# Performance work log

Measured on AMD Instinct MI355X. Metric: run time of the kernel, lower is better.

## Reference

```python
import jax, jax.numpy as jnp
import numpy as np

N_IN = 1024
N_OUT = 1024
BATCH = 8192
N_GRID = 10  # grid_points = linspace(-1, 1, 10); 9 segments
LN_EPS = 1e-5


def setup_inputs() -> dict:
    key = jax.random.key(0)
    k = jax.random.split(key, 6)
    return {
        "x": jax.random.normal(k[0], (BATCH, N_IN), dtype=jnp.float32),
        "weights": jax.random.normal(k[1], (N_OUT, N_IN), dtype=jnp.float32) * (1.0 / np.sqrt(N_IN)),
        "biases": jax.random.normal(k[2], (N_OUT,), dtype=jnp.float32),
        "slopes": jax.random.normal(k[3], (N_OUT, N_IN, N_GRID - 1), dtype=jnp.float32) * 0.05,
        "intercepts": jax.random.normal(k[4], (N_OUT, N_IN, N_GRID - 1), dtype=jnp.float32) * 0.05,
        "prelu_weight": jnp.full((1,), 0.25, dtype=jnp.float32),
    }


def reference(x, weights, biases, slopes, intercepts, prelu_weight):
    grid = jnp.linspace(-1.0, 1.0, N_GRID, dtype=x.dtype)
    n_seg = N_GRID - 1

    # base branch: GELU (exact, matching torch nn.GELU default) then linear
    b_out = jax.nn.gelu(x, approximate=False) @ weights.T + biases  # [B, n_out]

    # segment index per (sample, input feature)
    pos = (x[..., None] - grid) >= 0  # [B, n_in, N_GRID]
    seg = jnp.clip(jnp.sum(pos.astype(jnp.int32), axis=-1) - 1, 0, n_seg - 1)  # [B, n_in]

    # Faithful to torch.gather semantics: only slopes[:, 0, :] / intercepts[:, 0, :]
    # are read (index dim-2 has size 1 -> j==0). The piecewise sum over n_in then
    # reduces to segment-sums of x and segment counts contracted with those slices.
    onehot = jax.nn.one_hot(seg, n_seg, dtype=x.dtype)  # [B, n_in, n_seg]
    seg_x = jnp.einsum('bis,bi->bs', onehot, x)          # sum of x per segment
    seg_cnt = jnp.sum(onehot, axis=1)                    # count per segment
    slopes0 = slopes[:, 0, :]        # [n_out, n_seg]
    icpt0 = intercepts[:, 0, :]      # [n_out, n_seg]
    lin = seg_x @ slopes0.T + seg_cnt @ icpt0.T          # [B, n_out]

    y = b_out + lin
    # LayerNorm over n_out, no affine
    mu = jnp.mean(y, axis=-1, keepdims=True)
    var = jnp.mean(jnp.square(y - mu), axis=-1, keepdims=True)
    yn = (y - mu) * jax.lax.rsqrt(var + LN_EPS)
    # PReLU with single shared weight
    return jnp.where(yn >= 0, yn, prelu_weight * yn)
```

## Files before the change

### kernel.cpp

```cpp
#include <hip/hip_runtime.h>

#define N_IN 1024
#define N_OUT 1024
#define BATCHN 8192
#define BK 64

typedef __attribute__((ext_vector_type(8))) short short8;
typedef __attribute__((ext_vector_type(16))) float floatx16;

__device__ __forceinline__ unsigned short f2bf(float f) {
  unsigned int u = __float_as_uint(f);
  u += 0x7FFFu + ((u >> 16) & 1u);
  return (unsigned short)(u >> 16);
}
__device__ __forceinline__ float bf2f(unsigned short s) {
  return __uint_as_float(((unsigned int)s) << 16);
}

__global__ __launch_bounds__(256) void prep_all(const float* __restrict__ x,
                                                unsigned short* __restrict__ g,
                                                float* __restrict__ seg,
                                                const float* __restrict__ W,
                                                unsigned short* __restrict__ Wb,
                                                const float* __restrict__ slopes,
                                                const float* __restrict__ icpts,
                                                float* __restrict__ slt,
                                                float* __restrict__ ict) {
  const int b = blockIdx.x;
  const int t = threadIdx.x;
  if (b < BATCHN / 4) {
    const int lane = t & 63, wv = t >> 6;
    const int row = b * 4 + wv;
    const float* xr = x + row * N_IN;
    unsigned short* gr = g + row * N_IN;
    float cum[8], cumx[8], totx = 0.f;
#pragma unroll
    for (int s = 0; s < 8; ++s) { cum[s] = 0.f; cumx[s] = 0.f; }
#pragma unroll
    for (int j = 0; j < 4; ++j) {
      float4 v4 = ((const float4*)xr)[lane + 64 * j];
      float vs[4] = {v4.x, v4.y, v4.z, v4.w};
      ushort4 o4;
#pragma unroll
      for (int e = 0; e < 4; ++e) {
        float v = vs[e];
        float gl = 0.5f * v * (1.0f + erff(v * 0.70710678f));
        ((unsigned short*)&o4)[e] = f2bf(gl);
        totx += v;
#pragma unroll
        for (int k = 0; k < 8; ++k) {
          bool m = v >= (-1.0f + (float)(k + 1) * (2.0f / 9.0f));
          cum[k] += m ? 1.0f : 0.0f;
          cumx[k] += m ? v : 0.0f;
        }
      }
      ((ushort4*)gr)[lane + 64 * j] = o4;
    }
#pragma unroll
    for (int off = 32; off > 0; off >>= 1) {
      totx += __shfl_xor(totx, off);
#pragma unroll
      for (int s = 0; s < 8; ++s) {
        cum[s] += __shfl_xor(cum[s], off);
        cumx[s] += __shfl_xor(cumx[s], off);
      }
    }
    if (lane == 0) {
      float sx[9], sc[9];
      sx[0] = totx - cumx[0];
      sc[0] = 1024.f - cum[0];
#pragma unroll
      for (int s = 1; s < 8; ++s) {
        sx[s] = cumx[s - 1] - cumx[s];
        sc[s] = cum[s - 1] - cum[s];
      }
      sx[8] = cumx[7];
      sc[8] = cum[7];
#pragma unroll
      for (int s = 0; s < 9; ++s) {
        seg[row * 18 + s] = sx[s];
        seg[row * 18 + 9 + s] = sc[s];
      }
    }
  } else if (b < BATCHN / 4 + N_OUT) {
    const int o = b - BATCHN / 4;
    float4 v = ((const float4*)(W + o * N_IN))[t];
    ushort4 u;
    u.x = f2bf(v.x);
    u.y = f2bf(v.y);
    u.z = f2bf(v.z);
    u.w = f2bf(v.w);
    ((ushort4*)(Wb + o * N_IN))[t] = u;
  } else {
    const int gb = b - (BATCHN / 4 + N_OUT);
    const int o = gb * 16 + (t >> 4);
    const int s = t & 15;
    if (s < 9) {
      slt[s * N_OUT + o] = slopes[(long)o * 9216 + s];
      ict[s * N_OUT + o] = icpts[(long)o * 9216 + s];
    }
  }
}

#define ASYNC_CP16(gp, lp)                                                     \
  __builtin_amdgcn_global_load_lds(                                            \
      (const __attribute__((address_space(1))) unsigned int*)(gp),             \
      (__attribute__((address_space(3))) unsigned int*)(lp), 16, 0, 0)

__global__ __launch_bounds__(256) void gemm_bt(const unsigned short* __restrict__ A,
                                               const unsigned short* __restrict__ B,
                                               unsigned short* __restrict__ Cb) {
  __shared__ unsigned short lA[128 * BK];
  __shared__ unsigned short lB[128 * BK];
  const int t = threadIdx.x;
  const int m0 = blockIdx.x * 128;
  const int n0 = blockIdx.y * 128;
  const int lane = t & 63, wv = t >> 6;
  const int wm = (wv >> 1) * 64, wn = (wv & 1) * 64;
  floatx16 acc[2][2] = {};

  const int l31 = lane & 31;
  const int lh = lane >> 5;

  for (int kt = 0; kt < N_IN / BK; ++kt) {
    __syncthreads();
    const int ko = kt * BK;
#pragma unroll
    for (int j = 0; j < 4; ++j) {
      const int sg = t + 256 * j;
      const int r = sg >> 3;
      const int l = (sg & 7) ^ (r & 7);
      ASYNC_CP16(A + (m0 + r) * N_IN + ko + l * 8, &lA[sg * 8]);
    }
#pragma unroll
    for (int j = 0; j < 4; ++j) {
      const int sg = t + 256 * j;
      const int r = sg >> 3;
      const int l = (sg & 7) ^ (r & 7);
      ASYNC_CP16(B + (n0 + r) * N_IN + ko + l * 8, &lB[sg * 8]);
    }
    __syncthreads();
#pragma unroll
    for (int kk = 0; kk < 4; ++kk) {
      const int kc = kk * 2 + lh;
      short8 af[2], bf[2];
#pragma unroll
      for (int i = 0; i < 2; ++i) {
        const int row = wm + i * 32 + l31;
        af[i] = *(const short8*)&lA[row * BK + ((kc ^ (row & 7)) * 8)];
      }
#pragma unroll
      for (int i = 0; i < 2; ++i) {
        const int row = wn + i * 32 + l31;
        bf[i] = *(const short8*)&lB[row * BK + ((kc ^ (row & 7)) * 8)];
      }
#pragma unroll
      for (int mi = 0; mi < 2; ++mi)
#pragma unroll
        for (int ni = 0; ni < 2; ++ni)
          acc[mi][ni] = __builtin_amdgcn_mfma_f32_32x32x16_bf16(af[mi], bf[ni],
                                                                acc[mi][ni], 0, 0, 0);
    }
  }

  const int lrow = 4 * lh;
#pragma unroll
  for (int mi = 0; mi < 2; ++mi)
#pragma unroll
    for (int ni = 0; ni < 2; ++ni)
#pragma unroll
      for (int rg = 0; rg < 16; ++rg) {
        const int r = m0 + wm + mi * 32 + (rg & 3) + 8 * (rg >> 2) + lrow;
        const int c = n0 + wn + ni * 32 + l31;
        Cb[r * N_OUT + c] = f2bf(acc[mi][ni][rg]);
      }
}

__global__ __launch_bounds__(512) void ln_prelu(const unsigned short* __restrict__ Cb,
                                                float* __restrict__ out,
                                                const float* __restrict__ biases,
                                                const float* __restrict__ seg,
                                                const float* __restrict__ slt,
                                                const float* __restrict__ ict,
                                                const float* __restrict__ prelu_w) {
  const int t = threadIdx.x;
  const int o1 = t, o2 = t + 512;
  const int lane = t & 63, wv = t >> 6;
  const float b1 = biases[o1], b2 = biases[o2];
  float sl1[9], sl2[9], ic1[9], ic2[9];
#pragma unroll
  for (int s = 0; s < 9; ++s) {
    sl1[s] = slt[s * N_OUT + o1];
    sl2[s] = slt[s * N_OUT + o2];
    ic1[s] = ict[s * N_OUT + o1];
    ic2[s] = ict[s * N_OUT + o2];
  }
  const float pw = prelu_w[0];
  __shared__ float2 red[2][8];
  for (int r = 0; r < 8; ++r) {
    const int row = blockIdx.x * 8 + r;
    const float* segr = seg + row * 18;
    float y1 = bf2f(Cb[row * N_OUT + o1]) + b1;
    float y2 = bf2f(Cb[row * N_OUT + o2]) + b2;
#pragma unroll
    for (int s = 0; s < 9; ++s) {
      float sx = segr[s], ct = segr[9 + s];
      y1 += sx * sl1[s] + ct * ic1[s];
      y2 += sx * sl2[s] + ct * ic2[s];
    }
    float sum = y1 + y2;
    float sq = y1 * y1 + y2 * y2;
#pragma unroll
    for (int off = 32; off > 0; off >>= 1) {
      sum += __shfl_xor(sum, off);
      sq += __shfl_xor(sq, off);
    }
    if (lane == 0) red[r & 1][wv] = make_float2(sum, sq);
    __syncthreads();
    float s8 = 0.f, q8 = 0.f;
#pragma unroll
    for (int i = 0; i < 8; ++i) {
      s8 += red[r & 1][i].x;
      q8 += red[r & 1][i].y;
    }
    const float mu = s8 * (1.0f / 1024.0f);
    const float var = q8 * (1.0f / 1024.0f) - mu * mu;
    const float rstd = rsqrtf(var + 1e-5f);
    float z1 = (y1 - mu) * rstd, z2 = (y2 - mu) * rstd;
    z1 = z1 >= 0.f ? z1 : pw * z1;
    z2 = z2 >= 0.f ? z2 : pw * z2;
    out[row * N_OUT + o1] = z1;
    out[row * N_OUT + o2] = z2;
  }
}

extern "C" void kernel_launch(void* const* d_in, const int* in_sizes, int n_in,
                              void* d_out, int out_size, void* d_ws, size_t ws_size,
                              hipStream_t stream) {
  const float* x = (const float*)d_in[0];
  const float* W = (const float*)d_in[1];
  const float* biases = (const float*)d_in[2];
  const float* slopes = (const float*)d_in[3];
  const float* icpts = (const float*)d_in[4];
  const float* prelu_w = (const float*)d_in[5];
  float* out = (float*)d_out;

  char* ws = (char*)d_ws;
  unsigned short* g = (unsigned short*)ws;
  unsigned short* Wb = (unsigned short*)(ws + (16u << 20));
  unsigned short* Cb = (unsigned short*)(ws + (18u << 20));
  float* seg = (float*)(ws + (34u << 20));
  float* slt = (float*)(ws + (35u << 20));
  float* ict = (float*)(ws + (35u << 20) + (64u << 10));

  prep_all<<<BATCHN / 4 + N_OUT + 64, 256, 0, stream>>>(x, g, seg, W, Wb, slopes,
                                                        icpts, slt, ict);
  gemm_bt<<<dim3(BATCHN / 128, N_OUT / 128), 256, 0, stream>>>(g, Wb, Cb);
  ln_prelu<<<BATCHN / 8, 512, 0, stream>>>(Cb, out, biases, seg, slt, ict, prelu_w);
}
```

Baseline: 184.4 us.

## Switch GEMM operands to FP8 e4m3 with scaled MFMA

Quantizes GELU(x) and W to FP8 e4m3 with fixed power-of-two pre-scales, then runs the GEMM with the scaled 32x32x64 f8f6f4 MFMA, using block scales to undo the pre-scaling. This halves operand bytes and doubles the MFMA K per instruction, and the LDS tile grows to 128 bytes along K. The LayerNorm kernel also changes to contiguous paired loads and stores. The risk is accuracy loss from FP8 quantization of activations and weights against the tolerance.

```diff
diff --git a/kernel.cpp b/kernel.cpp
--- a/kernel.cpp
+++ b/kernel.cpp
@@ -1,11 +1,12 @@
 #include <hip/hip_runtime.h>
+#include <hip/hip_fp8.h>
 
 #define N_IN 1024
 #define N_OUT 1024
 #define BATCHN 8192
-#define BK 64
-
-typedef __attribute__((ext_vector_type(8))) short short8;
+
+typedef __attribute__((ext_vector_type(4))) int intx4;
+typedef __attribute__((ext_vector_type(8))) int intx8;
 typedef __attribute__((ext_vector_type(16))) float floatx16;
 
 __device__ __forceinline__ unsigned short f2bf(float f) {
@@ -16,12 +17,16 @@
 __device__ __forceinline__ float bf2f(unsigned short s) {
   return __uint_as_float(((unsigned int)s) << 16);
 }
+__device__ __forceinline__ unsigned int f2e4m3(float f) {
+  __hip_fp8_e4m3 v(f);
+  return (unsigned int)v.__x;
+}
 
 __global__ __launch_bounds__(256) void prep_all(const float* __restrict__ x,
-                                                unsigned short* __restrict__ g,
+                                                unsigned char* __restrict__ g8,
                                                 float* __restrict__ seg,
                                                 const float* __restrict__ W,
-                                                unsigned short* __restrict__ Wb,
+                                                unsigned char* __restrict__ Wb8,
                                                 const float* __restrict__ slopes,
                                                 const float* __restrict__ icpts,
                                                 float* __restrict__ slt,
@@ -32,7 +37,7 @@
     const int lane = t & 63, wv = t >> 6;
     const int row = b * 4 + wv;
     const float* xr = x + row * N_IN;
-    unsigned short* gr = g + row * N_IN;
+    unsigned int* gr = (unsigned int*)(g8 + row * N_IN);
     float cum[8], cumx[8], totx = 0.f;
 #pragma unroll
     for (int s = 0; s < 8; ++s) { cum[s] = 0.f; cumx[s] = 0.f; }
@@ -40,12 +45,12 @@
     for (int j = 0; j < 4; ++j) {
       float4 v4 = ((const float4*)xr)[lane + 64 * j];
       float vs[4] = {v4.x, v4.y, v4.z, v4.w};
-      ushort4 o4;
+      unsigned int pk = 0;
 #pragma unroll
       for (int e = 0; e < 4; ++e) {
         float v = vs[e];
         float gl = 0.5f * v * (1.0f + erff(v * 0.70710678f));
-        ((unsigned short*)&o4)[e] = f2bf(gl);
+        pk |= f2e4m3(gl * 4.0f) << (8 * e);
         totx += v;
 #pragma unroll
         for (int k = 0; k < 8; ++k) {
@@ -54,7 +59,7 @@
           cumx[k] += m ? v : 0.0f;
         }
       }
-      ((ushort4*)gr)[lane + 64 * j] = o4;
+      gr[lane + 64 * j] = pk;
     }
 #pragma unroll
     for (int off = 32; off > 0; off >>= 1) {
@@ -85,12 +90,9 @@
   } else if (b < BATCHN / 4 + N_OUT) {
     const int o = b - BATCHN / 4;
     float4 v = ((const float4*)(W + o * N_IN))[t];
-    ushort4 u;
-    u.x = f2bf(v.x);
-    u.y = f2bf(v.y);
-    u.z = f2bf(v.z);
-    u.w = f2bf(v.w);
-    ((ushort4*)(Wb + o * N_IN))[t] = u;
+    unsigned int pk = f2e4m3(v.x * 16.0f) | (f2e4m3(v.y * 16.0f) << 8) |
+                      (f2e4m3(v.z * 16.0f) << 16) | (f2e4m3(v.w * 16.0f) << 24);
+    ((unsigned int*)(Wb8 + o * N_IN))[t] = pk;
   } else {
     const int gb = b - (BATCHN / 4 + N_OUT);
     const int o = gb * 16 + (t >> 4);
@@ -107,11 +109,11 @@
       (const __attribute__((address_space(1))) unsigned int*)(gp),             \
       (__attribute__((address_space(3))) unsigned int*)(lp), 16, 0, 0)
 
-__global__ __launch_bounds__(256) void gemm_bt(const unsigned short* __restrict__ A,
-                                               const unsigned short* __restrict__ B,
+__global__ __launch_bounds__(256) void gemm_bt(const unsigned char* __restrict__ A,
+                                               const unsigned char* __restrict__ B,
                                                unsigned short* __restrict__ Cb) {
-  __shared__ unsigned short lA[128 * BK];
-  __shared__ unsigned short lB[128 * BK];
+  __shared__ unsigned char lA[128 * 128];
+  __shared__ unsigned char lB[128 * 128];
   const int t = threadIdx.x;
   const int m0 = blockIdx.x * 128;
   const int n0 = blockIdx.y * 128;
@@ -122,44 +124,53 @@
   const int l31 = lane & 31;
   const int lh = lane >> 5;
 
-  for (int kt = 0; kt < N_IN / BK; ++kt) {
+  for (int kt = 0; kt < N_IN / 128; ++kt) {
     __syncthreads();
-    const int ko = kt * BK;
+    const int ko = kt * 128;
 #pragma unroll
     for (int j = 0; j < 4; ++j) {
       const int sg = t + 256 * j;
       const int r = sg >> 3;
-      const int l = (sg & 7) ^ (r & 7);
-      ASYNC_CP16(A + (m0 + r) * N_IN + ko + l * 8, &lA[sg * 8]);
+      const int lc = (sg & 7) ^ (r & 7);
+      ASYNC_CP16(A + (m0 + r) * N_IN + ko + lc * 16, &lA[sg * 16]);
     }
 #pragma unroll
     for (int j = 0; j < 4; ++j) {
       const int sg = t + 256 * j;
       const int r = sg >> 3;
-      const int l = (sg & 7) ^ (r & 7);
-      ASYNC_CP16(B + (n0 + r) * N_IN + ko + l * 8, &lB[sg * 8]);
+      const int lc = (sg & 7) ^ (r & 7);
+      ASYNC_CP16(B + (n0 + r) * N_IN + ko + lc * 16, &lB[sg * 16]);
     }
     __syncthreads();
 #pragma unroll
-    for (int kk = 0; kk < 4; ++kk) {
-      const int kc = kk * 2 + lh;
-      short8 af[2], bf[2];
+    for (int kk = 0; kk < 2; ++kk) {
+      const int lc0 = kk * 4 + lh * 2;
+      intx8 af[2], bf[2];
 #pragma unroll
       for (int i = 0; i < 2; ++i) {
         const int row = wm + i * 32 + l31;
-        af[i] = *(const short8*)&lA[row * BK + ((kc ^ (row & 7)) * 8)];
+        const int sw = row & 7;
+        intx4 lo = *(const intx4*)&lA[row * 128 + ((lc0 ^ sw) * 16)];
+        intx4 hi = *(const intx4*)&lA[row * 128 + (((lc0 + 1) ^ sw) * 16)];
+        af[i][0] = lo[0]; af[i][1] = lo[1]; af[i][2] = lo[2]; af[i][3] = lo[3];
+        af[i][4] = hi[0]; af[i][5] = hi[1]; af[i][6] = hi[2]; af[i][7] = hi[3];
       }
 #pragma unroll
       for (int i = 0; i < 2; ++i) {
         const int row = wn + i * 32 + l31;
-        bf[i] = *(const short8*)&lB[row * BK + ((kc ^ (row & 7)) * 8)];
+        const int sw = row & 7;
+        intx4 lo = *(const intx4*)&lB[row * 128 + ((lc0 ^ sw) * 16)];
+        intx4 hi = *(const intx4*)&lB[row * 128 + (((lc0 + 1) ^ sw) * 16)];
+        bf[i][0] = lo[0]; bf[i][1] = lo[1]; bf[i][2] = lo[2]; bf[i][3] = lo[3];
+        bf[i][4] = hi[0]; bf[i][5] = hi[1]; bf[i][6] = hi[2]; bf[i][7] = hi[3];
       }
 #pragma unroll
       for (int mi = 0; mi < 2; ++mi)
 #pragma unroll
         for (int ni = 0; ni < 2; ++ni)
-          acc[mi][ni] = __builtin_amdgcn_mfma_f32_32x32x16_bf16(af[mi], bf[ni],
-                                                                acc[mi][ni], 0, 0, 0);
+          acc[mi][ni] = __builtin_amdgcn_mfma_scale_f32_32x32x64_f8f6f4(
+              af[mi], bf[ni], acc[mi][ni], 0 , 0 ,
+              0, 0x7D7D7D7Du , 0, 0x7B7B7B7Bu );
     }
   }
 
@@ -184,24 +195,25 @@
                                                 const float* __restrict__ ict,
                                                 const float* __restrict__ prelu_w) {
   const int t = threadIdx.x;
-  const int o1 = t, o2 = t + 512;
+  const int o = 2 * t;
   const int lane = t & 63, wv = t >> 6;
-  const float b1 = biases[o1], b2 = biases[o2];
+  const float b1 = biases[o], b2 = biases[o + 1];
   float sl1[9], sl2[9], ic1[9], ic2[9];
 #pragma unroll
   for (int s = 0; s < 9; ++s) {
-    sl1[s] = slt[s * N_OUT + o1];
-    sl2[s] = slt[s * N_OUT + o2];
-    ic1[s] = ict[s * N_OUT + o1];
-    ic2[s] = ict[s * N_OUT + o2];
+    sl1[s] = slt[s * N_OUT + o];
+    sl2[s] = slt[s * N_OUT + o + 1];
+    ic1[s] = ict[s * N_OUT + o];
+    ic2[s] = ict[s * N_OUT + o + 1];
   }
   const float pw = prelu_w[0];
   __shared__ float2 red[2][8];
   for (int r = 0; r < 8; ++r) {
     const int row = blockIdx.x * 8 + r;
     const float* segr = seg + row * 18;
-    float y1 = bf2f(Cb[row * N_OUT + o1]) + b1;
-    float y2 = bf2f(Cb[row * N_OUT + o2]) + b2;
+    ushort2 cc = *(const ushort2*)&Cb[row * N_OUT + o];
+    float y1 = bf2f(cc.x) + b1;
+    float y2 = bf2f(cc.y) + b2;
 #pragma unroll
     for (int s = 0; s < 9; ++s) {
       float sx = segr[s], ct = segr[9 + s];
@@ -229,8 +241,7 @@
     float z1 = (y1 - mu) * rstd, z2 = (y2 - mu) * rstd;
     z1 = z1 >= 0.f ? z1 : pw * z1;
     z2 = z2 >= 0.f ? z2 : pw * z2;
-    out[row * N_OUT + o1] = z1;
-    out[row * N_OUT + o2] = z2;
+    *(float2*)&out[row * N_OUT + o] = make_float2(z1, z2);
   }
 }
 
@@ -246,15 +257,15 @@
   float* out = (float*)d_out;
 
   char* ws = (char*)d_ws;
-  unsigned short* g = (unsigned short*)ws;
-  unsigned short* Wb = (unsigned short*)(ws + (16u << 20));
-  unsigned short* Cb = (unsigned short*)(ws + (18u << 20));
-  float* seg = (float*)(ws + (34u << 20));
-  float* slt = (float*)(ws + (35u << 20));
-  float* ict = (float*)(ws + (35u << 20) + (64u << 10));
-
-  prep_all<<<BATCHN / 4 + N_OUT + 64, 256, 0, stream>>>(x, g, seg, W, Wb, slopes,
+  unsigned char* g8 = (unsigned char*)ws;
+  unsigned char* Wb8 = (unsigned char*)(ws + (8u << 20));
+  unsigned short* Cb = (unsigned short*)(ws + (16u << 20));
+  float* seg = (float*)(ws + (33u << 20));
+  float* slt = (float*)(ws + (34u << 20));
+  float* ict = (float*)(ws + (34u << 20) + (64u << 10));
+
+  prep_all<<<BATCHN / 4 + N_OUT + 64, 256, 0, stream>>>(x, g8, seg, W, Wb8, slopes,
                                                         icpts, slt, ict);
-  gemm_bt<<<dim3(BATCHN / 128, N_OUT / 128), 256, 0, stream>>>(g, Wb, Cb);
+  gemm_bt<<<dim3(BATCHN / 128, N_OUT / 128), 256, 0, stream>>>(g8, Wb8, Cb);
   ln_prelu<<<BATCHN / 8, 512, 0, stream>>>(Cb, out, biases, seg, slt, ict, prelu_w);
 }
```

After: 175.8 us. 4.7% less time.
